# Kernel tuning notes

Hardware: AMD Instinct MI355X
Metric: run time of the kernel (lower is better)

## Reference

```python
import jax, jax.numpy as jnp
import numpy as np

NUM_EXPERTS = 8
TOP_K = 2
CAPACITY_FACTOR = 1.25
D_MODEL = 2048
HIDDEN = 2048
N_TOKENS = 4096


def _expert_capacity(n_tokens):
    ideal = TOP_K * n_tokens / NUM_EXPERTS
    allowed = int(CAPACITY_FACTOR * ideal)
    return ((allowed + 7) // 8) * 8  # ensure_multiple_of(..., 8)


def setup_inputs() -> dict:
    key = jax.random.key(0)
    ks = jax.random.split(key, 6)
    x = jax.random.normal(ks[0], (N_TOKENS, D_MODEL), dtype=jnp.float32)
    ew = jax.random.uniform(ks[1], (N_TOKENS, TOP_K), dtype=jnp.float32)
    expert_weights = ew / jnp.sum(ew, axis=-1, keepdims=True)  # router softmax-like weights
    expert_indices = jax.random.randint(ks[2], (N_TOKENS, TOP_K), 0, NUM_EXPERTS, dtype=jnp.int32)
    s = 1.0 / np.sqrt(D_MODEL)
    w1 = jax.random.normal(ks[3], (NUM_EXPERTS, D_MODEL, HIDDEN), dtype=jnp.float32) * s
    w3 = jax.random.normal(ks[4], (NUM_EXPERTS, D_MODEL, HIDDEN), dtype=jnp.float32) * s
    w2 = jax.random.normal(ks[5], (NUM_EXPERTS, HIDDEN, D_MODEL), dtype=jnp.float32) * (1.0 / np.sqrt(HIDDEN))
    return {"x": x, "expert_weights": expert_weights, "expert_indices": expert_indices,
            "w1": w1, "w2": w2, "w3": w3}


def reference(x, expert_weights, expert_indices, w1, w2, w3):
    N, d = x.shape
    E = NUM_EXPERTS
    cap = _expert_capacity(N)
    T = N * TOP_K

    flat_e = expert_indices.reshape(-1)                      # [T]
    # histc: tokens per expert
    counts = jnp.zeros((E,), jnp.int32).at[flat_e].add(1)
    # stable sort by expert id (torch.sort on ints is stable here semantically)
    order = jnp.argsort(flat_e, stable=True)                 # [T]
    sorted_e = flat_e[order]
    starts = jnp.cumsum(counts) - counts                     # bin start offsets
    pos = jnp.arange(T, dtype=jnp.int32) - starts[sorted_e]  # rank within expert bin
    valid = pos < cap                                        # drop tokens over capacity
    tok = order // TOP_K                                     # source token per routed slot

    # binned_gather -> [E, cap, d]
    dest = jnp.where(valid, sorted_e * cap + pos, 0)
    xg = jnp.zeros((E * cap, d), x.dtype).at[dest].add(
        jnp.where(valid[:, None], x[tok], 0.0))
    xg = xg.reshape(E, cap, d)

    # grouped SwiGLU MLP per expert
    h = jax.nn.silu(jnp.einsum('ecd,edh->ech', xg, w1)) * jnp.einsum('ecd,edh->ech', xg, w3)
    ye = jnp.einsum('ech,ehd->ecd', h, w2).reshape(E * cap, d)

    # binned_scatter with expert weights (combine)
    w_flat = expert_weights.reshape(-1)[order]               # [T]
    contrib = ye[dest] * (w_flat * valid.astype(x.dtype))[:, None]
    y = jnp.zeros((N, d), x.dtype).at[tok].add(contrib)
    return y, counts
```

## Files before the change

### kernel.cpp

```cpp
#include <hip/hip_runtime.h>
#include <cstdint>

#define NEXP 8
#define TOPK 2
#define NTOK 4096
#define NSLOT (NTOK * TOPK)
#define CAP 1280
#define DM 2048
#define EC (NEXP * CAP)

typedef __bf16 bf16x8 __attribute__((ext_vector_type(8)));
typedef float  f32x4  __attribute__((ext_vector_type(4)));
typedef int    i32x4  __attribute__((ext_vector_type(4)));
typedef int    i32x8  __attribute__((ext_vector_type(8)));

typedef const void __attribute__((address_space(1))) gvoid;
typedef void __attribute__((address_space(3))) lvoid;

__device__ __forceinline__ void gld16(const void* g, void* l) {
  __builtin_amdgcn_global_load_lds((gvoid*)(uintptr_t)g, (lvoid*)(uintptr_t)l,
                                   16, 0, 0);
}

__device__ __forceinline__ unsigned fp8x4(float a, float b, float c, float d) {
  int v = __builtin_amdgcn_cvt_pk_fp8_f32(a, b, 0, false);
  v = __builtin_amdgcn_cvt_pk_fp8_f32(c, d, v, true);
  return (unsigned)v;
}
__device__ __forceinline__ unsigned char fp8one(float a) {
  return (unsigned char)(__builtin_amdgcn_cvt_pk_fp8_f32(a, a, 0, false) & 0xff);
}

__global__ void route_k(const int* __restrict__ eidx, int* __restrict__ row_token,
                        int* __restrict__ slot_dest, int* __restrict__ mcount,
                        float* __restrict__ out) {
  __shared__ int lh[256][NEXP];
  int tid = threadIdx.x;
  for (int i = tid; i < EC; i += 256) row_token[i] = -1;
#pragma unroll
  for (int e = 0; e < NEXP; ++e) lh[tid][e] = 0;
  __syncthreads();
  int base = tid * 32;
  for (int j = 0; j < 32; ++j) lh[tid][eidx[base + j]]++;
  __syncthreads();
  if (tid < NEXP) {
    int run = 0;
    for (int i = 0; i < 256; ++i) { int t = lh[i][tid]; lh[i][tid] = run; run += t; }
    mcount[tid] = run < CAP ? run : CAP;
    out[(size_t)NTOK * DM + tid] = (float)run;
  }
  __syncthreads();
  for (int j = 0; j < 32; ++j) {
    int t = base + j;
    int e = eidx[t];
    int r = lh[tid][e]++;
    if (r < CAP) { int dst = e * CAP + r; slot_dest[t] = dst; row_token[dst] = t >> 1; }
    else slot_dest[t] = -1;
  }
}

__global__ void gather_k(const float* __restrict__ x, const int* __restrict__ row_token,
                         unsigned char* __restrict__ xg) {
  int r = blockIdx.x;
  int c = threadIdx.x * 8;
  int tok = row_token[r];
  uint2 o;
  if (tok >= 0) {
    const float* src = x + (size_t)tok * DM + c;
    float4 a = *(const float4*)src;
    float4 b = *(const float4*)(src + 4);
    o.x = fp8x4(a.x, a.y, a.z, a.w);
    o.y = fp8x4(b.x, b.y, b.z, b.w);
  } else {
    o.x = 0u; o.y = 0u;
  }
  *(uint2*)(xg + (size_t)r * DM + c) = o;
}

__global__ void transT_k(const float* __restrict__ w, unsigned char* __restrict__ wT) {
  __shared__ float t[64][69];
  int e = blockIdx.z;
  int n0 = blockIdx.x * 64, k0 = blockIdx.y * 64;
  const float* src = w + ((size_t)e << 22) + (size_t)k0 * DM + n0;
  unsigned char* dst = wT + ((size_t)e << 22) + (size_t)n0 * DM + k0;
  int c4 = (threadIdx.x & 15) * 4, r0 = threadIdx.x >> 4;
#pragma unroll
  for (int p = 0; p < 4; ++p) {
    int r = p * 16 + r0;
    float4 v = *(const float4*)(src + (size_t)r * DM + c4);
    t[r][c4 + 0] = v.x; t[r][c4 + 1] = v.y; t[r][c4 + 2] = v.z; t[r][c4 + 3] = v.w;
  }
  __syncthreads();
  int j = threadIdx.x & 7, rr0 = threadIdx.x >> 3;
#pragma unroll
  for (int q = 0; q < 2; ++q) {
    int rr = q * 32 + rr0;
    int k8 = j * 8;
    uint2 v;
    v.x = fp8x4(t[k8 + 0][rr], t[k8 + 1][rr], t[k8 + 2][rr], t[k8 + 3][rr]);
    v.y = fp8x4(t[k8 + 4][rr], t[k8 + 5][rr], t[k8 + 6][rr], t[k8 + 7][rr]);
    *(uint2*)(dst + (size_t)rr * DM + k8) = v;
  }
}

__global__ __launch_bounds__(256, 2)
void gemm13_k(const unsigned char* __restrict__ A0, const unsigned char* __restrict__ B1T,
              const unsigned char* __restrict__ B3T, unsigned char* __restrict__ H,
              const int* __restrict__ mcount) {
  int lbid = blockIdx.x + 16 * (blockIdx.y + 10 * blockIdx.z);
  int nb = (lbid & 7) * 160 + (lbid >> 3);
  int e = nb / 160, rem = nb % 160, mt = rem >> 4, nt = rem & 15;
  int mc = mcount[e];
  if (mt * 128 >= mc) return;

  __shared__ __align__(16) char smem[48 * 1024];
  char* lA  = smem;
  char* lB1 = smem + 16384;
  char* lB3 = smem + 32768;

  int row0 = e * CAP + mt * 128;
  const unsigned char* gA  = A0 + (size_t)row0 * DM;
  size_t boff = ((size_t)e * DM + (size_t)nt * 128) * DM;
  const unsigned char* gB1 = B1T + boff;
  const unsigned char* gB3 = B3T + boff;

  int tid = threadIdx.x, w = tid >> 6, l = tid & 63;
  int wr = w >> 1, wc = w & 1;
  int lr = l & 15, kg = l >> 4;

  int sr = tid >> 3;
  int scs = (tid & 7) ^ (sr & 7);

  f32x4 acc1[4][4], acc3[4][4];
#pragma unroll
  for (int m = 0; m < 4; ++m)
#pragma unroll
    for (int n = 0; n < 4; ++n)
#pragma unroll
      for (int j = 0; j < 4; ++j) { acc1[m][n][j] = 0.f; acc3[m][n][j] = 0.f; }

  auto rdfrag = [&](const char* lX, int R) -> i32x8 {
    int r = R + lr;
    int a0 = r * 128 + (((2 * kg + 0) ^ (r & 7)) << 4);
    int a1 = r * 128 + (((2 * kg + 1) ^ (r & 7)) << 4);
    i32x4 lo = *(const i32x4*)(lX + a0);
    i32x4 hi = *(const i32x4*)(lX + a1);
    i32x8 v;
    v[0] = lo[0]; v[1] = lo[1]; v[2] = lo[2]; v[3] = lo[3];
    v[4] = hi[0]; v[5] = hi[1]; v[6] = hi[2]; v[7] = hi[3];
    return v;
  };

#pragma unroll 1
  for (int ks = 0; ks < 16; ++ks) {
#pragma unroll
    for (int s = 0; s < 4; ++s) {
      size_t goff = (size_t)(s * 32 + sr) * DM + (size_t)ks * 128 + scs * 16;
      gld16(gA  + goff, lA  + s * 4096 + w * 1024);
      gld16(gB1 + goff, lB1 + s * 4096 + w * 1024);
      gld16(gB3 + goff, lB3 + s * 4096 + w * 1024);
    }
    __syncthreads();
    i32x8 bf1[4], bf3[4];
#pragma unroll
    for (int n = 0; n < 4; ++n) bf1[n] = rdfrag(lB1, wc * 64 + n * 16);
#pragma unroll
    for (int n = 0; n < 4; ++n) bf3[n] = rdfrag(lB3, wc * 64 + n * 16);
#pragma unroll
    for (int m = 0; m < 4; ++m) {
      i32x8 af = rdfrag(lA, wr * 64 + m * 16);
#pragma unroll
      for (int n = 0; n < 4; ++n)
        acc1[m][n] = __builtin_amdgcn_mfma_scale_f32_16x16x128_f8f6f4(
            af, bf1[n], acc1[m][n], 0, 0, 0, 0x7F, 0, 0x7F);
#pragma unroll
      for (int n = 0; n < 4; ++n)
        acc3[m][n] = __builtin_amdgcn_mfma_scale_f32_16x16x128_f8f6f4(
            af, bf3[n], acc3[m][n], 0, 0, 0, 0x7F, 0, 0x7F);
    }
    __syncthreads();
  }

  int rg = l >> 4;
#pragma unroll
  for (int m = 0; m < 4; ++m)
#pragma unroll
    for (int n = 0; n < 4; ++n)
#pragma unroll
      for (int j = 0; j < 4; ++j) {
        int rr = row0 + wr * 64 + m * 16 + rg * 4 + j;
        int cc = nt * 128 + wc * 64 + n * 16 + lr;
        float u = acc1[m][n][j];
        float s = u / (1.f + __expf(-u));
        H[(size_t)rr * DM + cc] = fp8one(s * acc3[m][n][j]);
      }
}

__global__ __launch_bounds__(256, 4)
void gemm_k(const unsigned char* __restrict__ A0, const unsigned char* __restrict__ BT,
            __bf16* __restrict__ C, const int* __restrict__ mcount) {
  int lbid = blockIdx.x + 16 * (blockIdx.y + 10 * blockIdx.z);
  int nb = (lbid & 7) * 160 + (lbid >> 3);
  int e = nb / 160, rem = nb % 160, mt = rem >> 4, nt = rem & 15;
  int mc = mcount[e];
  if (mt * 128 >= mc) return;

  __shared__ __align__(16) char smem[32 * 1024];
  char* lA = smem;
  char* lB = smem + 16384;

  int row0 = e * CAP + mt * 128;
  const unsigned char* gA = A0 + (size_t)row0 * DM;
  const unsigned char* gB = BT + ((size_t)e * DM + (size_t)nt * 128) * DM;

  int tid = threadIdx.x, w = tid >> 6, l = tid & 63;
  int wr = w >> 1, wc = w & 1;
  int lr = l & 15, kg = l >> 4;

  int sr = tid >> 3;
  int scs = (tid & 7) ^ (sr & 7);

  f32x4 acc[4][4];
#pragma unroll
  for (int m = 0; m < 4; ++m)
#pragma unroll
    for (int n = 0; n < 4; ++n)
#pragma unroll
      for (int j = 0; j < 4; ++j) acc[m][n][j] = 0.f;

  auto rdfrag = [&](const char* lX, int R) -> i32x8 {
    int r = R + lr;
    int a0 = r * 128 + (((2 * kg + 0) ^ (r & 7)) << 4);
    int a1 = r * 128 + (((2 * kg + 1) ^ (r & 7)) << 4);
    i32x4 lo = *(const i32x4*)(lX + a0);
    i32x4 hi = *(const i32x4*)(lX + a1);
    i32x8 v;
    v[0] = lo[0]; v[1] = lo[1]; v[2] = lo[2]; v[3] = lo[3];
    v[4] = hi[0]; v[5] = hi[1]; v[6] = hi[2]; v[7] = hi[3];
    return v;
  };

#pragma unroll 1
  for (int ks = 0; ks < 16; ++ks) {
#pragma unroll
    for (int s = 0; s < 4; ++s) {
      size_t goff = (size_t)(s * 32 + sr) * DM + (size_t)ks * 128 + scs * 16;
      gld16(gA + goff, lA + s * 4096 + w * 1024);
      gld16(gB + goff, lB + s * 4096 + w * 1024);
    }
    __syncthreads();
    i32x8 bf[4];
#pragma unroll
    for (int n = 0; n < 4; ++n) bf[n] = rdfrag(lB, wc * 64 + n * 16);
#pragma unroll
    for (int m = 0; m < 4; ++m) {
      i32x8 af = rdfrag(lA, wr * 64 + m * 16);
#pragma unroll
      for (int n = 0; n < 4; ++n)
        acc[m][n] = __builtin_amdgcn_mfma_scale_f32_16x16x128_f8f6f4(
            af, bf[n], acc[m][n], 0, 0, 0, 0x7F, 0, 0x7F);
    }
    __syncthreads();
  }

  int rg = l >> 4;
#pragma unroll
  for (int m = 0; m < 4; ++m)
#pragma unroll
    for (int n = 0; n < 4; ++n)
#pragma unroll
      for (int j = 0; j < 4; ++j) {
        int rr = row0 + wr * 64 + m * 16 + rg * 4 + j;
        int cc = nt * 128 + wc * 64 + n * 16 + lr;
        C[(size_t)rr * DM + cc] = (__bf16)acc[m][n][j];
      }
}

__global__ void combine_k(const __bf16* __restrict__ ye, const int* __restrict__ slot_dest,
                          const float* __restrict__ ew, float* __restrict__ out) {
  int tok = blockIdx.x;
  int c = threadIdx.x * 8;
  int d0 = slot_dest[2 * tok], d1 = slot_dest[2 * tok + 1];
  float w0 = ew[2 * tok], w1 = ew[2 * tok + 1];
  float r[8];
#pragma unroll
  for (int j = 0; j < 8; ++j) r[j] = 0.f;
  if (d0 >= 0) {
    bf16x8 y0 = *(const bf16x8*)(ye + (size_t)d0 * DM + c);
#pragma unroll
    for (int j = 0; j < 8; ++j) r[j] += w0 * (float)y0[j];
  }
  if (d1 >= 0) {
    bf16x8 y1 = *(const bf16x8*)(ye + (size_t)d1 * DM + c);
#pragma unroll
    for (int j = 0; j < 8; ++j) r[j] += w1 * (float)y1[j];
  }
  float* dst = out + (size_t)tok * DM + c;
  float4 o0; o0.x = r[0]; o0.y = r[1]; o0.z = r[2]; o0.w = r[3];
  float4 o1; o1.x = r[4]; o1.y = r[5]; o1.z = r[6]; o1.w = r[7];
  *(float4*)dst = o0;
  *(float4*)(dst + 4) = o1;
}

extern "C" void kernel_launch(void* const* d_in, const int* in_sizes, int n_in,
                              void* d_out, int out_size, void* d_ws, size_t ws_size,
                              hipStream_t stream) {
  const float* x  = (const float*)d_in[0];
  const float* ew = (const float*)d_in[1];
  const int*   ei = (const int*)d_in[2];
  const float* w1 = (const float*)d_in[3];
  const float* w2 = (const float*)d_in[4];
  const float* w3 = (const float*)d_in[5];
  float* out = (float*)d_out;
  char* ws = (char*)d_ws;

  const size_t SZ8  = (size_t)EC * DM;
  const size_t SZ16 = 2 * SZ8;
  const size_t SZW  = (size_t)NEXP * DM * DM;
  unsigned char* xg  = (unsigned char*)ws;
  __bf16* yeB        = (__bf16*)(ws + SZ8);
  unsigned char* hB  = (unsigned char*)(ws + SZ8 + SZ16);
  unsigned char* wT1 = (unsigned char*)(ws + 2 * SZ8 + SZ16);
  unsigned char* wT3 = (unsigned char*)(ws + 2 * SZ8 + SZ16 + SZW);
  char* ints = ws + 2 * SZ8 + SZ16 + 2 * SZW;
  int* row_token = (int*)ints;
  int* slot_dest = row_token + EC;
  int* mcount    = slot_dest + NSLOT;

  dim3 tgrid(32, 32, NEXP);
  dim3 ggrid(16, 10, NEXP);

  route_k<<<1, 256, 0, stream>>>(ei, row_token, slot_dest, mcount, out);
  gather_k<<<EC, 256, 0, stream>>>(x, row_token, xg);

  transT_k<<<tgrid, 256, 0, stream>>>(w1, wT1);
  transT_k<<<tgrid, 256, 0, stream>>>(w3, wT3);
  gemm13_k<<<ggrid, 256, 0, stream>>>(xg, wT1, wT3, hB, mcount);

  transT_k<<<tgrid, 256, 0, stream>>>(w2, wT1);
  gemm_k<<<ggrid, 256, 0, stream>>>(hB, wT1, yeB, mcount);

  combine_k<<<NTOK, 256, 0, stream>>>(yeB, slot_dest, ew, out);
}
```

Baseline: 303.6 us.

## Merge weight transposes and gather into fused launches overlapping GEMM

Merges the w1/w3 transpose-to-fp8 kernels and the token gather into one prep kernel, and appends the w2 transpose blocks to the gate/up GEMM launch, writing them to a separate workspace buffer. This cuts the number of launches and lets the w2 conversion overlap the first GEMM instead of running serially between the GEMMs. In exchange, the GEMM kernel now reserves 48KB of LDS for transpose blocks, the workspace grows by one weight copy, and block scheduling order decides how much overlap actually happens.

```diff
diff --git a/kernel.cpp b/kernel.cpp
--- a/kernel.cpp
+++ b/kernel.cpp
@@ -59,28 +59,10 @@
   }
 }
 
-__global__ void gather_k(const float* __restrict__ x, const int* __restrict__ row_token,
-                         unsigned char* __restrict__ xg) {
-  int r = blockIdx.x;
-  int c = threadIdx.x * 8;
-  int tok = row_token[r];
-  uint2 o;
-  if (tok >= 0) {
-    const float* src = x + (size_t)tok * DM + c;
-    float4 a = *(const float4*)src;
-    float4 b = *(const float4*)(src + 4);
-    o.x = fp8x4(a.x, a.y, a.z, a.w);
-    o.y = fp8x4(b.x, b.y, b.z, b.w);
-  } else {
-    o.x = 0u; o.y = 0u;
-  }
-  *(uint2*)(xg + (size_t)r * DM + c) = o;
-}
-
-__global__ void transT_k(const float* __restrict__ w, unsigned char* __restrict__ wT) {
-  __shared__ float t[64][69];
-  int e = blockIdx.z;
-  int n0 = blockIdx.x * 64, k0 = blockIdx.y * 64;
+__device__ __forceinline__ void transT_tile(const float* __restrict__ w,
+                                            unsigned char* __restrict__ wT,
+                                            int e, int n0, int k0, char* smem) {
+  float (*t)[69] = (float (*)[69])smem;
   const float* src = w + ((size_t)e << 22) + (size_t)k0 * DM + n0;
   unsigned char* dst = wT + ((size_t)e << 22) + (size_t)n0 * DM + k0;
   int c4 = (threadIdx.x & 15) * 4, r0 = threadIdx.x >> 4;
@@ -103,17 +85,57 @@
   }
 }
 
+__global__ __launch_bounds__(256)
+void prep_k(const float* __restrict__ w1, const float* __restrict__ w3,
+            unsigned char* __restrict__ wT1, unsigned char* __restrict__ wT3,
+            const float* __restrict__ x, const int* __restrict__ row_token,
+            unsigned char* __restrict__ xg) {
+  __shared__ __align__(16) char smem[64 * 69 * 4];
+  int bid = blockIdx.x;
+  if (bid < 16384) {
+    const float* w = (bid & 8192) ? w3 : w1;
+    unsigned char* wT = (bid & 8192) ? wT3 : wT1;
+    int rem = bid & 8191;
+    int e = rem >> 10, t = rem & 1023;
+    transT_tile(w, wT, e, (t & 31) * 64, (t >> 5) * 64, smem);
+  } else {
+    int rbase = (bid - 16384) * 8;
+    int c = threadIdx.x * 8;
+#pragma unroll 1
+    for (int i = 0; i < 8; ++i) {
+      int r = rbase + i;
+      int tok = row_token[r];
+      uint2 o;
+      if (tok >= 0) {
+        const float* src = x + (size_t)tok * DM + c;
+        float4 a = *(const float4*)src;
+        float4 b = *(const float4*)(src + 4);
+        o.x = fp8x4(a.x, a.y, a.z, a.w);
+        o.y = fp8x4(b.x, b.y, b.z, b.w);
+      } else { o.x = 0u; o.y = 0u; }
+      *(uint2*)(xg + (size_t)r * DM + c) = o;
+    }
+  }
+}
+
 __global__ __launch_bounds__(256, 2)
-void gemm13_k(const unsigned char* __restrict__ A0, const unsigned char* __restrict__ B1T,
-              const unsigned char* __restrict__ B3T, unsigned char* __restrict__ H,
-              const int* __restrict__ mcount) {
-  int lbid = blockIdx.x + 16 * (blockIdx.y + 10 * blockIdx.z);
+void gemm13t_k(const unsigned char* __restrict__ A0, const unsigned char* __restrict__ B1T,
+               const unsigned char* __restrict__ B3T, unsigned char* __restrict__ H,
+               const int* __restrict__ mcount,
+               const float* __restrict__ w2, unsigned char* __restrict__ wT2) {
+  __shared__ __align__(16) char smem[48 * 1024];
+  if (blockIdx.x >= 1280) {
+    int rem = blockIdx.x - 1280;
+    int e = rem >> 10, t = rem & 1023;
+    transT_tile(w2, wT2, e, (t & 31) * 64, (t >> 5) * 64, smem);
+    return;
+  }
+  int lbid = blockIdx.x;
   int nb = (lbid & 7) * 160 + (lbid >> 3);
   int e = nb / 160, rem = nb % 160, mt = rem >> 4, nt = rem & 15;
   int mc = mcount[e];
   if (mt * 128 >= mc) return;
 
-  __shared__ __align__(16) char smem[48 * 1024];
   char* lA  = smem;
   char* lB1 = smem + 16384;
   char* lB3 = smem + 32768;
@@ -322,23 +344,17 @@
   unsigned char* hB  = (unsigned char*)(ws + SZ8 + SZ16);
   unsigned char* wT1 = (unsigned char*)(ws + 2 * SZ8 + SZ16);
   unsigned char* wT3 = (unsigned char*)(ws + 2 * SZ8 + SZ16 + SZW);
-  char* ints = ws + 2 * SZ8 + SZ16 + 2 * SZW;
+  unsigned char* wT2 = (unsigned char*)(ws + 2 * SZ8 + SZ16 + 2 * SZW);
+  char* ints = ws + 2 * SZ8 + SZ16 + 3 * SZW;
   int* row_token = (int*)ints;
   int* slot_dest = row_token + EC;
   int* mcount    = slot_dest + NSLOT;
 
-  dim3 tgrid(32, 32, NEXP);
   dim3 ggrid(16, 10, NEXP);
 
   route_k<<<1, 256, 0, stream>>>(ei, row_token, slot_dest, mcount, out);
-  gather_k<<<EC, 256, 0, stream>>>(x, row_token, xg);
-
-  transT_k<<<tgrid, 256, 0, stream>>>(w1, wT1);
-  transT_k<<<tgrid, 256, 0, stream>>>(w3, wT3);
-  gemm13_k<<<ggrid, 256, 0, stream>>>(xg, wT1, wT3, hB, mcount);
-
-  transT_k<<<tgrid, 256, 0, stream>>>(w2, wT1);
-  gemm_k<<<ggrid, 256, 0, stream>>>(hB, wT1, yeB, mcount);
-
+  prep_k<<<17664, 256, 0, stream>>>(w1, w3, wT1, wT3, x, row_token, xg);
+  gemm13t_k<<<9472, 256, 0, stream>>>(xg, wT1, wT3, hB, mcount, w2, wT2);
+  gemm_k<<<ggrid, 256, 0, stream>>>(hB, wT2, yeB, mcount);
   combine_k<<<NTOK, 256, 0, stream>>>(yeB, slot_dest, ew, out);
 }
```

After: 265.6 us (median of 2 runs). 12.5% less time.
